# Kernel optimization log

Hardware: AMD Instinct MI355X
Metric: run time of the kernel (lower is better)

The kernel has to match this reference:

```python
import jax, jax.numpy as jnp
import numpy as np

HIDDEN = 1024
K_ALIVE = 9          # CodebookConfig.initial_size; alive_mask[:9] = True in __init__
MAX_SIZE = 64
INIT_SCALE = 0.02
DENSITY = 0.05       # SynaptogenesisConfig.initial_density
TAU = 0.07
LN_EPS = 1e-5
NORM_EPS = 1e-12     # F.normalize default eps


def setup_inputs() -> dict:
    key = jax.random.key(0)
    k_h, k_w, k_m, k_p = jax.random.split(key, 4)
    h = jax.random.normal(k_h, (8, 4096, HIDDEN), dtype=jnp.float32)
    weight = jax.random.normal(k_w, (HIDDEN, HIDDEN), dtype=jnp.float32) * 0.02
    mask = (jax.random.uniform(k_m, (HIDDEN, HIDDEN)) < DENSITY).astype(jnp.float32)
    prototypes = jax.random.normal(k_p, (MAX_SIZE, HIDDEN), dtype=jnp.float32) * INIT_SCALE
    gamma = jnp.ones((HIDDEN,), dtype=jnp.float32)   # LayerNorm weight
    beta = jnp.zeros((HIDDEN,), dtype=jnp.float32)   # LayerNorm bias
    return {"h": h, "weight": weight, "mask": mask, "gamma": gamma,
            "beta": beta, "prototypes": prototypes}


def _l2norm(x):
    n = jnp.linalg.norm(x, axis=-1, keepdims=True)
    return x / jnp.maximum(n, NORM_EPS)


def reference(h, weight, mask, gamma, beta, prototypes):
    # SparseSynapticLayer: F.linear(h, weight * mask)  [B,S,D] @ [D,D]^T
    z = jnp.einsum('bsd,od->bso', h, weight * mask)
    # LayerNorm over last dim
    mu = jnp.mean(z, axis=-1, keepdims=True)
    var = jnp.mean(jnp.square(z - mu), axis=-1, keepdims=True)
    z = (z - mu) * jax.lax.rsqrt(var + LN_EPS) * gamma + beta
    # DynamicActionCodebook: cosine similarity to alive prototypes / tau
    live = prototypes[:K_ALIVE]            # alive_mask = first K_ALIVE slots
    logits = jnp.einsum('bsd,kd->bsk', _l2norm(z), _l2norm(live)) / TAU
    return logits, z
```

## Files before the change

### kernel.cpp

```cpp
#include <hip/hip_runtime.h>
#include <stdint.h>

#define HIDDEN 1024
#define MROWS  32768
#define NPROTO 9
#define ZOFF   (MROWS * NPROTO)

typedef __bf16 bf16x8 __attribute__((ext_vector_type(8)));
typedef float  f32x4  __attribute__((ext_vector_type(4)));

__device__ __forceinline__ unsigned short f2bf(float f) {
    unsigned u = __float_as_uint(f);
    u += 0x7fffu + ((u >> 16) & 1u);
    return (unsigned short)(u >> 16);
}
__device__ __forceinline__ float bf2f(unsigned short u) {
    return __uint_as_float(((unsigned)u) << 16);
}

__global__ void k_conv_w(const float* __restrict__ w, const float* __restrict__ m,
                         unsigned short* __restrict__ dst, int n8) {
    int i0 = blockIdx.x * blockDim.x + threadIdx.x;
    int stride = gridDim.x * blockDim.x;
    for (int i = i0; i < n8; i += stride) {
        const float4* pw = (const float4*)(w + (size_t)i * 8);
        const float4* pm = (const float4*)(m + (size_t)i * 8);
        float4 a = pw[0], b = pw[1], c = pm[0], d = pm[1];
        union { unsigned short us[8]; uint4 v; } o;
        o.us[0] = f2bf(a.x * c.x); o.us[1] = f2bf(a.y * c.y);
        o.us[2] = f2bf(a.z * c.z); o.us[3] = f2bf(a.w * c.w);
        o.us[4] = f2bf(b.x * d.x); o.us[5] = f2bf(b.y * d.y);
        o.us[6] = f2bf(b.z * d.z); o.us[7] = f2bf(b.w * d.w);
        *(uint4*)(dst + (size_t)i * 8) = o.v;
    }
}

__global__ void k_proto(const float* __restrict__ proto, float* __restrict__ pn) {
    __shared__ float red[4];
    int t = threadIdx.x, k = blockIdx.x;
    float4 v = *(const float4*)(proto + (size_t)k * HIDDEN + t * 4);
    float ss = v.x * v.x + v.y * v.y + v.z * v.z + v.w * v.w;
    #pragma unroll
    for (int m = 1; m < 64; m <<= 1) ss += __shfl_xor(ss, m);
    if ((t & 63) == 0) red[t >> 6] = ss;
    __syncthreads();
    ss = red[0] + red[1] + red[2] + red[3];
    float inv = 1.0f / fmaxf(sqrtf(ss), 1e-12f);
    float4 o; o.x = v.x * inv; o.y = v.y * inv; o.z = v.z * inv; o.w = v.w * inv;
    *(float4*)(pn + (size_t)k * HIDDEN + t * 4) = o;
}

__global__ __launch_bounds__(256, 2) void k_gemm(const float* __restrict__ H,
                                                 const unsigned short* __restrict__ B,
                                                 unsigned short* __restrict__ ZP) {
    __shared__ unsigned short As[2][128 * 32];
    __shared__ unsigned short Bs[2][128 * 32];
    const int tid = threadIdx.x;
    const int wid = tid >> 6, lane = tid & 63;
    const int hw = (int)blockIdx.x;
    const int xcd = hw & 7, nblk = (hw >> 3) & 7, mloc = hw >> 6;
    const int bm0 = (xcd * 32 + mloc) * 128;
    const int bn0 = nblk * 128;
    const int wr = wid >> 1, wc = wid & 1;
    const int fr = lane & 15, kq = lane >> 4;

    const int arow = tid >> 1, ahalf = tid & 1;
    const float* ha = H + (size_t)(bm0 + arow) * HIDDEN + ahalf * 16;

    f32x4 acc[4][4] = {};

    auto loadA = [&](float4* f, int k0) {
        const float4* p = (const float4*)(ha + k0);
        #pragma unroll
        for (int q = 0; q < 4; q++) f[q] = p[q];
    };
    auto writeA = [&](int buf, const float4* f) {
        union { unsigned short us[16]; uint4 v[2]; } o;
        #pragma unroll
        for (int q = 0; q < 4; q++) {
            o.us[q * 4 + 0] = f2bf(f[q].x); o.us[q * 4 + 1] = f2bf(f[q].y);
            o.us[q * 4 + 2] = f2bf(f[q].z); o.us[q * 4 + 3] = f2bf(f[q].w);
        }
        uint4* dst = (uint4*)&As[buf][arow * 32 + ahalf * 16];
        dst[0] = o.v[0];
        dst[1] = o.v[1];
    };
    auto stageB = [&](int buf, int k0) {
        #pragma unroll
        for (int is = 0; is < 2; ++is) {
            int c = is * 256 + tid;
            int row = c >> 2, seg = c & 3;
            const unsigned short* gb = B + (size_t)(bn0 + row) * HIDDEN + k0 + seg * 8;
            void* lb = (void*)((char*)&Bs[buf][0] + (size_t)(is * 256 + wid * 64) * 16);
            __builtin_amdgcn_global_load_lds((const __attribute__((address_space(1))) void*)gb,
                                             (__attribute__((address_space(3))) void*)lb, 16, 0, 0);
        }
    };
    auto compute = [&](int buf) {
        bf16x8 av[4], bv[4];
        #pragma unroll
        for (int i = 0; i < 4; i++)
            av[i] = *(const bf16x8*)&As[buf][(wr * 64 + i * 16 + fr) * 32 + kq * 8];
        #pragma unroll
        for (int j = 0; j < 4; j++)
            bv[j] = *(const bf16x8*)&Bs[buf][(wc * 64 + j * 16 + fr) * 32 + kq * 8];
        #pragma unroll
        for (int i = 0; i < 4; i++)
            #pragma unroll
            for (int j = 0; j < 4; j++)
                acc[i][j] = __builtin_amdgcn_mfma_f32_16x16x32_bf16(av[i], bv[j], acc[i][j], 0, 0, 0);
    };

    float4 af[4];
    loadA(af, 0);
    stageB(0, 0);
    writeA(0, af);
    __syncthreads();
    int cur = 0;
    for (int t = 1; t < 32; t++) {
        float4 an[4];
        loadA(an, t * 32);
        stageB(cur ^ 1, t * 32);
        compute(cur);
        writeA(cur ^ 1, an);
        __syncthreads();
        cur ^= 1;
    }
    compute(cur);

    #pragma unroll
    for (int i = 0; i < 4; i++) {
        #pragma unroll
        for (int j = 0; j < 4; j++) {
            int col = bn0 + wc * 64 + j * 16 + fr;
            int rowb = bm0 + wr * 64 + i * 16 + kq * 4;
            #pragma unroll
            for (int r = 0; r < 4; r++)
                ZP[(size_t)(rowb + r) * HIDDEN + col] = f2bf(acc[i][j][r]);
        }
    }
}

__global__ __launch_bounds__(256) void k_ln(const unsigned short* __restrict__ zp,
                                            float* __restrict__ z, float* __restrict__ logits,
                                            const float* __restrict__ gamma, const float* __restrict__ beta,
                                            const float* __restrict__ pn, int waves_total) {
    __shared__ float sp[NPROTO * HIDDEN];
    const int tid = threadIdx.x, wid = tid >> 6, lane = tid & 63;
    #pragma unroll
    for (int i = 0; i < NPROTO * HIDDEN / 4 / 256; i++) {
        int idx = (i * 256 + tid) * 4;
        *(float4*)&sp[idx] = *(const float4*)&pn[idx];
    }
    __syncthreads();

    float4 g4[4], b4[4];
    #pragma unroll
    for (int c = 0; c < 4; c++) {
        g4[c] = *(const float4*)(gamma + lane * 4 + 256 * c);
        b4[c] = *(const float4*)(beta  + lane * 4 + 256 * c);
    }

    const float inv_n = 1.0f / 1024.0f;
    int gw = blockIdx.x * 4 + wid;
    for (int row = gw; row < MROWS; row += waves_total) {
        const unsigned short* zr = zp + (size_t)row * HIDDEN;
        float4 v[4];
        #pragma unroll
        for (int c = 0; c < 4; c++) {
            ushort4 u = *(const ushort4*)(zr + lane * 4 + 256 * c);
            v[c].x = bf2f(u.x); v[c].y = bf2f(u.y); v[c].z = bf2f(u.z); v[c].w = bf2f(u.w);
        }

        float s = 0.f, sq = 0.f;
        #pragma unroll
        for (int c = 0; c < 4; c++) {
            s  += v[c].x + v[c].y + v[c].z + v[c].w;
            sq += v[c].x * v[c].x + v[c].y * v[c].y + v[c].z * v[c].z + v[c].w * v[c].w;
        }
        #pragma unroll
        for (int m = 1; m < 64; m <<= 1) { s += __shfl_xor(s, m); sq += __shfl_xor(sq, m); }

        float mu  = s * inv_n;
        float var = sq * inv_n - mu * mu;
        float rs  = rsqrtf(var + 1e-5f);

        float* zo = z + (size_t)row * HIDDEN;
        #pragma unroll
        for (int c = 0; c < 4; c++) {
            v[c].x = (v[c].x - mu) * rs * g4[c].x + b4[c].x;
            v[c].y = (v[c].y - mu) * rs * g4[c].y + b4[c].y;
            v[c].z = (v[c].z - mu) * rs * g4[c].z + b4[c].z;
            v[c].w = (v[c].w - mu) * rs * g4[c].w + b4[c].w;
            *(float4*)(zo + lane * 4 + 256 * c) = v[c];
        }

        float part[10];
        #pragma unroll
        for (int k = 0; k < 10; k++) part[k] = 0.f;
        #pragma unroll
        for (int c = 0; c < 4; c++) {
            part[9] += v[c].x * v[c].x + v[c].y * v[c].y + v[c].z * v[c].z + v[c].w * v[c].w;
            #pragma unroll
            for (int k = 0; k < 9; k++) {
                float4 p = *(const float4*)&sp[k * HIDDEN + lane * 4 + 256 * c];
                part[k] += v[c].x * p.x + v[c].y * p.y + v[c].z * p.z + v[c].w * p.w;
            }
        }
        #pragma unroll
        for (int m = 1; m < 64; m <<= 1) {
            #pragma unroll
            for (int k = 0; k < 10; k++) part[k] += __shfl_xor(part[k], m);
        }
        if (lane == 0) {
            float inv = 1.0f / (fmaxf(sqrtf(part[9]), 1e-12f) * 0.07f);
            #pragma unroll
            for (int k = 0; k < 9; k++) logits[(size_t)row * NPROTO + k] = part[k] * inv;
        }
    }
}

extern "C" void kernel_launch(void* const* d_in, const int* in_sizes, int n_in,
                              void* d_out, int out_size, void* d_ws, size_t ws_size,
                              hipStream_t stream) {
    const float* h     = (const float*)d_in[0];
    const float* w     = (const float*)d_in[1];
    const float* mask  = (const float*)d_in[2];
    const float* gamma = (const float*)d_in[3];
    const float* beta  = (const float*)d_in[4];
    const float* proto = (const float*)d_in[5];
    float* out    = (float*)d_out;
    float* logits = out;
    float* z      = out + (size_t)ZOFF;

    char* ws = (char*)d_ws;
    unsigned short* zp = (unsigned short*)ws;
    unsigned short* wm = (unsigned short*)(ws + 67108864);
    float*          pn = (float*)(ws + 67108864 + 2097152);

    k_conv_w<<<512, 256, 0, stream>>>(w, mask, wm, HIDDEN * HIDDEN / 8);
    k_proto<<<NPROTO, 256, 0, stream>>>(proto, pn);
    k_gemm<<<2048, 256, 0, stream>>>(h, wm, zp);
    k_ln<<<2048, 256, 0, stream>>>(zp, z, logits, gamma, beta, pn, 2048 * 4);
}
```

Measured before the change: 201.7 us.

## Stage fp32 A tiles directly to LDS with swizzle, convert to bf16 at fragment load

The A operand (fp32 activations) is now copied global-to-LDS with async global_load_lds instead of going through registers, where it was converted to bf16 and written back to LDS. An XOR swizzle on 16-byte chunks is applied to avoid LDS bank conflicts. The bf16 conversion moves into the compute step, where each wave reads fp32 from LDS. This frees VGPRs and removes register round-trips, letting the loads overlap with MFMA work. The cost is double the LDS footprint (48KB), which may hurt occupancy at 2 blocks/CU, more LDS read bandwidth, and per-use conversion done redundantly across the two column waves. The conversion also changes from the custom round-to-nearest-even helper to the compiler's __bf16 cast.

```diff
diff --git a/kernel.cpp b/kernel.cpp
--- a/kernel.cpp
+++ b/kernel.cpp
@@ -53,8 +53,7 @@
 __global__ __launch_bounds__(256, 2) void k_gemm(const float* __restrict__ H,
                                                  const unsigned short* __restrict__ B,
                                                  unsigned short* __restrict__ ZP) {
-    __shared__ unsigned short As[2][128 * 32];
-    __shared__ unsigned short Bs[2][128 * 32];
+    __shared__ char smem[49152];
     const int tid = threadIdx.x;
     const int wid = tid >> 6, lane = tid & 63;
     const int hw = (int)blockIdx.x;
@@ -64,26 +63,19 @@
     const int wr = wid >> 1, wc = wid & 1;
     const int fr = lane & 15, kq = lane >> 4;
 
-    const int arow = tid >> 1, ahalf = tid & 1;
-    const float* ha = H + (size_t)(bm0 + arow) * HIDDEN + ahalf * 16;
-
     f32x4 acc[4][4] = {};
 
-    auto loadA = [&](float4* f, int k0) {
-        const float4* p = (const float4*)(ha + k0);
-        #pragma unroll
-        for (int q = 0; q < 4; q++) f[q] = p[q];
-    };
-    auto writeA = [&](int buf, const float4* f) {
-        union { unsigned short us[16]; uint4 v[2]; } o;
-        #pragma unroll
-        for (int q = 0; q < 4; q++) {
-            o.us[q * 4 + 0] = f2bf(f[q].x); o.us[q * 4 + 1] = f2bf(f[q].y);
-            o.us[q * 4 + 2] = f2bf(f[q].z); o.us[q * 4 + 3] = f2bf(f[q].w);
-        }
-        uint4* dst = (uint4*)&As[buf][arow * 32 + ahalf * 16];
-        dst[0] = o.v[0];
-        dst[1] = o.v[1];
+    auto stageA = [&](int buf, int k0) {
+        #pragma unroll
+        for (int it = 0; it < 4; ++it) {
+            int c = it * 256 + tid;
+            int row = c >> 3, ch = c & 7;
+            int g = ch ^ (row & 7);
+            const float* ga = H + (size_t)(bm0 + row) * HIDDEN + k0 + g * 4;
+            void* la = (void*)(smem + buf * 16384 + (size_t)(it * 256 + wid * 64) * 16);
+            __builtin_amdgcn_global_load_lds((const __attribute__((address_space(1))) void*)ga,
+                                             (__attribute__((address_space(3))) void*)la, 16, 0, 0);
+        }
     };
     auto stageB = [&](int buf, int k0) {
         #pragma unroll
@@ -91,19 +83,29 @@
             int c = is * 256 + tid;
             int row = c >> 2, seg = c & 3;
             const unsigned short* gb = B + (size_t)(bn0 + row) * HIDDEN + k0 + seg * 8;
-            void* lb = (void*)((char*)&Bs[buf][0] + (size_t)(is * 256 + wid * 64) * 16);
+            void* lb = (void*)(smem + 32768 + buf * 8192 + (size_t)(is * 256 + wid * 64) * 16);
             __builtin_amdgcn_global_load_lds((const __attribute__((address_space(1))) void*)gb,
                                              (__attribute__((address_space(3))) void*)lb, 16, 0, 0);
         }
     };
+
     auto compute = [&](int buf) {
+        const char* as = smem + buf * 16384;
+        const unsigned short* bs = (const unsigned short*)(smem + 32768 + buf * 8192);
         bf16x8 av[4], bv[4];
         #pragma unroll
-        for (int i = 0; i < 4; i++)
-            av[i] = *(const bf16x8*)&As[buf][(wr * 64 + i * 16 + fr) * 32 + kq * 8];
+        for (int i = 0; i < 4; i++) {
+            int r = wr * 64 + i * 16 + fr;
+            f32x4 lo = *(const f32x4*)(as + r * 128 + (((2 * kq)     ^ (fr & 7)) * 16));
+            f32x4 hi = *(const f32x4*)(as + r * 128 + (((2 * kq + 1) ^ (fr & 7)) * 16));
+            bf16x8 a;
+            a[0] = (__bf16)lo[0]; a[1] = (__bf16)lo[1]; a[2] = (__bf16)lo[2]; a[3] = (__bf16)lo[3];
+            a[4] = (__bf16)hi[0]; a[5] = (__bf16)hi[1]; a[6] = (__bf16)hi[2]; a[7] = (__bf16)hi[3];
+            av[i] = a;
+        }
         #pragma unroll
         for (int j = 0; j < 4; j++)
-            bv[j] = *(const bf16x8*)&Bs[buf][(wc * 64 + j * 16 + fr) * 32 + kq * 8];
+            bv[j] = *(const bf16x8*)&bs[(wc * 64 + j * 16 + fr) * 32 + kq * 8];
         #pragma unroll
         for (int i = 0; i < 4; i++)
             #pragma unroll
@@ -111,18 +113,14 @@
                 acc[i][j] = __builtin_amdgcn_mfma_f32_16x16x32_bf16(av[i], bv[j], acc[i][j], 0, 0, 0);
     };
 
-    float4 af[4];
-    loadA(af, 0);
+    stageA(0, 0);
     stageB(0, 0);
-    writeA(0, af);
     __syncthreads();
     int cur = 0;
     for (int t = 1; t < 32; t++) {
-        float4 an[4];
-        loadA(an, t * 32);
+        stageA(cur ^ 1, t * 32);
         stageB(cur ^ 1, t * 32);
         compute(cur);
-        writeA(cur ^ 1, an);
         __syncthreads();
         cur ^= 1;
     }
```

Result: faster. 193.1 us (-4.3%).
